# Kernel tuning notes

Hardware: AMD Instinct MI355X
Metric: run time of the kernel (lower is better)

The kernel has to match this reference:

```python
import jax, jax.numpy as jnp
import numpy as np

B, T, D_IN, EMB, H = 2, 2048, 1024, 1024, 16
HD = EMB // H  # head_dim = 64


def setup_inputs() -> dict:
    key = jax.random.key(0)
    ks = jax.random.split(key, 3)
    scale_qkv = 1.0 / np.sqrt(D_IN)
    scale_o = 1.0 / np.sqrt(EMB)
    return {
        "x": jax.random.normal(ks[0], (B, T, D_IN), dtype=jnp.float32),
        "W_qkv": jax.random.normal(ks[1], (D_IN, 3 * EMB), dtype=jnp.float32) * scale_qkv,
        "b_qkv": jnp.zeros((3 * EMB,), dtype=jnp.float32),
        "W_o": jax.random.normal(ks[2], (EMB, EMB), dtype=jnp.float32) * scale_o,
        "b_o": jnp.zeros((EMB,), dtype=jnp.float32),
    }


def reference(x, W_qkv, b_qkv, W_o, b_o):
    b, t, _ = x.shape
    qkv = x @ W_qkv + b_qkv                      # [B,T,3*EMB]
    # Match torch: reshape to (B,T,H,3*HD) -> permute -> chunk into q,k,v
    qkv = qkv.reshape(b, t, H, 3 * HD).transpose(0, 2, 1, 3)  # [B,H,T,3*HD]
    q, k, v = jnp.split(qkv, 3, axis=-1)         # each [B,H,T,HD]
    scale = 1.0 / jnp.sqrt(jnp.asarray(HD, dtype=q.dtype))
    scores = jnp.einsum("bhqd,bhkd->bhqk", q, k) * scale  # [B,H,T,T]
    attn = jax.nn.softmax(scores, axis=-1)
    values = jnp.einsum("bhqk,bhkd->bhqd", attn, v)       # [B,H,T,HD]
    values = values.transpose(0, 2, 1, 3).reshape(b, t, EMB)
    return values @ W_o + b_o
```

## Files before the change

kernel.cpp:

```cpp
#include <hip/hip_runtime.h>
#include <math.h>

typedef __bf16 bf16x8 __attribute__((ext_vector_type(8)));
typedef float f32x4 __attribute__((ext_vector_type(4)));

#define GPTR(p) ((const __attribute__((address_space(1))) void*)(p))
#define LPTR(p) ((__attribute__((address_space(3))) void*)(p))

#define QSCALE 0.18033688011112042f

__device__ __forceinline__ unsigned short f2bf(float f) {
  unsigned int u = __float_as_uint(f);
  u += 0x7FFFu + ((u >> 16) & 1u);
  return (unsigned short)(u >> 16);
}

__device__ __forceinline__ unsigned int pack_bf2(float lo, float hi) {
  return __builtin_amdgcn_perm(__float_as_uint(hi) + 0x8000u,
                               __float_as_uint(lo) + 0x8000u, 0x07060302u);
}

__device__ __forceinline__ float fast_exp2(float x) {
#if __has_builtin(__builtin_amdgcn_exp2f)
  return __builtin_amdgcn_exp2f(x);
#else
  return exp2f(x);
#endif
}

__device__ __forceinline__ f32x4 zero4() {
  f32x4 z; z[0] = 0.f; z[1] = 0.f; z[2] = 0.f; z[3] = 0.f; return z;
}

__global__ void conv_x_bf16(const float* __restrict__ in, unsigned short* __restrict__ out) {
  int i = (blockIdx.x * 256 + threadIdx.x) * 4;
  float4 v = *(const float4*)(in + i);
  ushort4 o;
  o.x = f2bf(v.x); o.y = f2bf(v.y); o.z = f2bf(v.z); o.w = f2bf(v.w);
  *(ushort4*)(out + i) = o;
}

__global__ void transpose_conv(const float* __restrict__ in, unsigned short* __restrict__ out,
                               int K, int N) {
  __shared__ float tile[64][65];
  int k0 = blockIdx.y * 64, n0 = blockIdx.x * 64;
  int t = threadIdx.x;
#pragma unroll
  for (int p = 0; p < 16; ++p) {
    int l = p * 256 + t; int r = l >> 6, c = l & 63;
    tile[r][c] = in[(size_t)(k0 + r) * N + n0 + c];
  }
  __syncthreads();
#pragma unroll
  for (int p = 0; p < 16; ++p) {
    int l = p * 256 + t; int r = l >> 6, c = l & 63;
    out[(size_t)(n0 + r) * K + k0 + c] = f2bf(tile[c][r]);
  }
}

__global__ __launch_bounds__(256) void gemm_qkv(
    const unsigned short* __restrict__ A, const unsigned short* __restrict__ Bt,
    const float* __restrict__ bias,
    unsigned short* __restrict__ Qd, unsigned short* __restrict__ Kd,
    unsigned short* __restrict__ Vtd) {
  __shared__ unsigned short As[128 * 32];
  __shared__ unsigned short Bs[128 * 32];
  const int tid = threadIdx.x, wave = tid >> 6, lane = tid & 63;
  const int quad = lane >> 4, l16 = lane & 15;
  const int wm = (wave >> 1) * 64, wn = (wave & 1) * 64;
  const int m0 = blockIdx.y * 128, n0 = blockIdx.x * 128;
  f32x4 acc[4][4];
#pragma unroll
  for (int i = 0; i < 4; ++i)
#pragma unroll
    for (int j = 0; j < 4; ++j) acc[i][j] = zero4();

  const int c = wave * 64 + lane;
  const int rA = c >> 2, o16 = (c & 3) * 8;

  for (int k0 = 0; k0 < 1024; k0 += 32) {
    __syncthreads();
    __builtin_amdgcn_global_load_lds(GPTR(A + (size_t)(m0 + rA) * 1024 + k0 + o16),
                                     LPTR(As + wave * 512), 16, 0, 0);
    __builtin_amdgcn_global_load_lds(GPTR(A + (size_t)(m0 + 64 + rA) * 1024 + k0 + o16),
                                     LPTR(As + 2048 + wave * 512), 16, 0, 0);
    __builtin_amdgcn_global_load_lds(GPTR(Bt + (size_t)(n0 + rA) * 1024 + k0 + o16),
                                     LPTR(Bs + wave * 512), 16, 0, 0);
    __builtin_amdgcn_global_load_lds(GPTR(Bt + (size_t)(n0 + 64 + rA) * 1024 + k0 + o16),
                                     LPTR(Bs + 2048 + wave * 512), 16, 0, 0);
    __syncthreads();
    bf16x8 af[4], bfr[4];
#pragma unroll
    for (int mt = 0; mt < 4; ++mt)
      af[mt] = *(const bf16x8*)(As + (wm + mt * 16 + l16) * 32 + quad * 8);
#pragma unroll
    for (int nt = 0; nt < 4; ++nt)
      bfr[nt] = *(const bf16x8*)(Bs + (wn + nt * 16 + l16) * 32 + quad * 8);
#pragma unroll
    for (int mt = 0; mt < 4; ++mt)
#pragma unroll
      for (int nt = 0; nt < 4; ++nt)
        acc[mt][nt] = __builtin_amdgcn_mfma_f32_16x16x32_bf16(af[mt], bfr[nt], acc[mt][nt], 0, 0, 0);
  }

#pragma unroll
  for (int mt = 0; mt < 4; ++mt) {
#pragma unroll
    for (int nt = 0; nt < 4; ++nt) {
      int m = m0 + wm + mt * 16 + quad * 4;
      int n = n0 + wn + nt * 16 + l16;
      float bv = bias[n];
      int h = n / 192, rem = n - h * 192;
      int which = rem >> 6, d = rem & 63;
      int b = m >> 11, t0 = m & 2047;
      size_t head = (size_t)(b * 16 + h);
      f32x4 a = acc[mt][nt];
      if (which == 0) {
        size_t base = (head * 2048 + t0) * 64 + d;
#pragma unroll
        for (int i = 0; i < 4; ++i)
          Qd[base + (size_t)i * 64] = f2bf((a[i] + bv) * QSCALE);
      } else if (which == 1) {
        size_t base = head * 131072 + (size_t)(t0 >> 6) * 4096;
#pragma unroll
        for (int i = 0; i < 4; ++i) {
          int tt = t0 + i;
          Kd[base + (tt & 63) * 64 + (((d >> 3) ^ (tt & 7)) << 3) + (d & 7)] = f2bf(a[i] + bv);
        }
      } else {
        size_t base = head * 131072 + (size_t)(t0 >> 6) * 4096;
        ushort4 o;
        o.x = f2bf(a[0] + bv); o.y = f2bf(a[1] + bv);
        o.z = f2bf(a[2] + bv); o.w = f2bf(a[3] + bv);
        *(ushort4*)(Vtd + base + d * 64 + (((((t0 & 63) >> 3)) ^ (d & 7)) << 3) + (t0 & 7)) = o;
      }
    }
  }
}

__global__ __launch_bounds__(256) void flash_attn(
    const unsigned short* __restrict__ Qg,
    const unsigned short* __restrict__ Kg,
    const unsigned short* __restrict__ Vg,
    unsigned short* __restrict__ att) {
  __shared__ unsigned short Ks[4096];
  __shared__ unsigned short Vs[4096];
  __shared__ unsigned short Ps[8192];
  const int tid = threadIdx.x, wave = tid >> 6, lane = tid & 63;
  const int quad = lane >> 4, l16 = lane & 15;
  const int h7 = l16 & 7;
  const int bh = blockIdx.y;
  const int q0 = blockIdx.x * 128 + wave * 32;

  bf16x8 bq[2][2];
#pragma unroll
  for (int qg = 0; qg < 2; ++qg)
#pragma unroll
    for (int kh = 0; kh < 2; ++kh)
      bq[qg][kh] = *(const bf16x8*)(Qg + ((size_t)bh * 2048 + q0 + qg * 16 + l16) * 64 + kh * 32 + quad * 8);

  f32x4 o[2][4];
#pragma unroll
  for (int qg = 0; qg < 2; ++qg)
#pragma unroll
    for (int i = 0; i < 4; ++i) o[qg][i] = zero4();
  float l_run[2] = {0.f, 0.f};

  unsigned short* pb = Ps + wave * 2048;
  const unsigned short* Kt = Kg + (size_t)bh * 131072;
  const unsigned short* Vt = Vg + (size_t)bh * 131072;

  for (int tile = 0; tile < 32; ++tile) {
    __syncthreads();
    const unsigned short* Kb = Kt + tile * 4096 + lane * 8;
    const unsigned short* Vb = Vt + tile * 4096 + lane * 8;
    __builtin_amdgcn_global_load_lds(GPTR(Kb + wave * 512),       LPTR(Ks + wave * 512), 16, 0, 0);
    __builtin_amdgcn_global_load_lds(GPTR(Kb + (4 + wave) * 512), LPTR(Ks + (4 + wave) * 512), 16, 0, 0);
    __builtin_amdgcn_global_load_lds(GPTR(Vb + wave * 512),       LPTR(Vs + wave * 512), 16, 0, 0);
    __builtin_amdgcn_global_load_lds(GPTR(Vb + (4 + wave) * 512), LPTR(Vs + (4 + wave) * 512), 16, 0, 0);
    __syncthreads();

    f32x4 s[2][4];
#pragma unroll
    for (int qg = 0; qg < 2; ++qg)
#pragma unroll
      for (int kt = 0; kt < 4; ++kt) s[qg][kt] = zero4();
#pragma unroll
    for (int kt = 0; kt < 4; ++kt) {
#pragma unroll
      for (int kh = 0; kh < 2; ++kh) {
        bf16x8 a = *(const bf16x8*)(Ks + (kt * 16 + l16) * 64 + (((kh * 4 + quad) ^ h7) << 3));
        s[0][kt] = __builtin_amdgcn_mfma_f32_16x16x32_bf16(a, bq[0][kh], s[0][kt], 0, 0, 0);
        s[1][kt] = __builtin_amdgcn_mfma_f32_16x16x32_bf16(a, bq[1][kh], s[1][kt], 0, 0, 0);
      }
    }

#pragma unroll
    for (int qg = 0; qg < 2; ++qg) {
      int qrow = qg * 16 + l16;
      float lsum = 0.f;
      float pv[4][4];
#pragma unroll
      for (int kt = 0; kt < 4; ++kt)
#pragma unroll
        for (int r = 0; r < 4; ++r) {
          float p = fast_exp2(s[qg][kt][r]);
          pv[kt][r] = p;
          lsum += p;
        }
#pragma unroll
      for (int kt = 0; kt < 4; ++kt) {
        uint2 pk;
        pk.x = pack_bf2(pv[kt][0], pv[kt][1]);
        pk.y = pack_bf2(pv[kt][2], pv[kt][3]);
        *(uint2*)(pb + qrow * 64 + (((2 * kt + (quad >> 1)) ^ h7) << 3) + (quad & 1) * 4) = pk;
      }
      lsum += __shfl_xor(lsum, 16);
      lsum += __shfl_xor(lsum, 32);
      l_run[qg] += lsum;
    }

#pragma unroll
    for (int st = 0; st < 2; ++st) {
      bf16x8 pf0 = *(const bf16x8*)(pb + (l16) * 64 + (((st * 4 + quad) ^ h7) << 3));
      bf16x8 pf1 = *(const bf16x8*)(pb + (16 + l16) * 64 + (((st * 4 + quad) ^ h7) << 3));
#pragma unroll
      for (int mt = 0; mt < 4; ++mt) {
        bf16x8 av = *(const bf16x8*)(Vs + (mt * 16 + l16) * 64 + (((st * 4 + quad) ^ h7) << 3));
        o[0][mt] = __builtin_amdgcn_mfma_f32_16x16x32_bf16(av, pf0, o[0][mt], 0, 0, 0);
        o[1][mt] = __builtin_amdgcn_mfma_f32_16x16x32_bf16(av, pf1, o[1][mt], 0, 0, 0);
      }
    }
  }

  int b = bh >> 4, h = bh & 15;
#pragma unroll
  for (int qg = 0; qg < 2; ++qg) {
    float inv_l = 1.f / l_run[qg];
    unsigned short* orow = att + ((size_t)b * 2048 + q0 + qg * 16 + l16) * 1024 + h * 64;
#pragma unroll
    for (int mt = 0; mt < 4; ++mt) {
      ushort4 ov;
      ov.x = f2bf(o[qg][mt][0] * inv_l);
      ov.y = f2bf(o[qg][mt][1] * inv_l);
      ov.z = f2bf(o[qg][mt][2] * inv_l);
      ov.w = f2bf(o[qg][mt][3] * inv_l);
      *(ushort4*)(orow + mt * 16 + quad * 4) = ov;
    }
  }
}

__global__ __launch_bounds__(256) void gemm_out(
    const unsigned short* __restrict__ A, const unsigned short* __restrict__ Bt,
    const float* __restrict__ bias, float* __restrict__ out) {
  __shared__ unsigned short As[128 * 32];
  __shared__ unsigned short Bs[64 * 32];
  const int tid = threadIdx.x, wave = tid >> 6, lane = tid & 63;
  const int quad = lane >> 4, l16 = lane & 15;
  const int wm = (wave >> 1) * 64, wn = (wave & 1) * 32;
  const int m0 = blockIdx.y * 128, n0 = blockIdx.x * 64;
  f32x4 acc[4][2];
#pragma unroll
  for (int i = 0; i < 4; ++i)
#pragma unroll
    for (int j = 0; j < 2; ++j) acc[i][j] = zero4();

  const int c = wave * 64 + lane;
  const int rA = c >> 2, o16 = (c & 3) * 8;

  for (int k0 = 0; k0 < 1024; k0 += 32) {
    __syncthreads();
    __builtin_amdgcn_global_load_lds(GPTR(A + (size_t)(m0 + rA) * 1024 + k0 + o16),
                                     LPTR(As + wave * 512), 16, 0, 0);
    __builtin_amdgcn_global_load_lds(GPTR(A + (size_t)(m0 + 64 + rA) * 1024 + k0 + o16),
                                     LPTR(As + 2048 + wave * 512), 16, 0, 0);
    __builtin_amdgcn_global_load_lds(GPTR(Bt + (size_t)(n0 + rA) * 1024 + k0 + o16),
                                     LPTR(Bs + wave * 512), 16, 0, 0);
    __syncthreads();
    bf16x8 af[4], bfr[2];
#pragma unroll
    for (int mt = 0; mt < 4; ++mt)
      af[mt] = *(const bf16x8*)(As + (wm + mt * 16 + l16) * 32 + quad * 8);
#pragma unroll
    for (int nt = 0; nt < 2; ++nt)
      bfr[nt] = *(const bf16x8*)(Bs + (wn + nt * 16 + l16) * 32 + quad * 8);
#pragma unroll
    for (int mt = 0; mt < 4; ++mt)
#pragma unroll
      for (int nt = 0; nt < 2; ++nt)
        acc[mt][nt] = __builtin_amdgcn_mfma_f32_16x16x32_bf16(af[mt], bfr[nt], acc[mt][nt], 0, 0, 0);
  }

#pragma unroll
  for (int mt = 0; mt < 4; ++mt) {
#pragma unroll
    for (int nt = 0; nt < 2; ++nt) {
      int m = m0 + wm + mt * 16 + quad * 4;
      int n = n0 + wn + nt * 16 + l16;
      float bv = bias[n];
      float* orow = out + (size_t)m * 1024 + n;
      orow[0]        = acc[mt][nt][0] + bv;
      orow[1024]     = acc[mt][nt][1] + bv;
      orow[2 * 1024] = acc[mt][nt][2] + bv;
      orow[3 * 1024] = acc[mt][nt][3] + bv;
    }
  }
}

extern "C" void kernel_launch(void* const* d_in, const int* in_sizes, int n_in,
                              void* d_out, int out_size, void* d_ws, size_t ws_size,
                              hipStream_t stream) {
  const float* x    = (const float*)d_in[0];
  const float* Wqkv = (const float*)d_in[1];
  const float* bqkv = (const float*)d_in[2];
  const float* Wo   = (const float*)d_in[3];
  const float* bo   = (const float*)d_in[4];
  float* out = (float*)d_out;

  unsigned short* xb    = (unsigned short*)d_ws;
  unsigned short* wqkvt = xb    + (size_t)4096 * 1024;
  unsigned short* wot   = wqkvt + (size_t)3072 * 1024;
  unsigned short* Qd    = wot   + (size_t)1024 * 1024;
  unsigned short* Kd    = Qd    + (size_t)32 * 2048 * 64;
  unsigned short* Vtd   = Kd    + (size_t)32 * 2048 * 64;
  unsigned short* attb  = Vtd   + (size_t)32 * 2048 * 64;

  conv_x_bf16<<<4096, 256, 0, stream>>>(x, xb);
  transpose_conv<<<dim3(48, 16), 256, 0, stream>>>(Wqkv, wqkvt, 1024, 3072);
  transpose_conv<<<dim3(16, 16), 256, 0, stream>>>(Wo, wot, 1024, 1024);
  gemm_qkv<<<dim3(24, 32), 256, 0, stream>>>(xb, wqkvt, bqkv, Qd, Kd, Vtd);
  flash_attn<<<dim3(16, 32), 256, 0, stream>>>(Qd, Kd, Vtd, attb);
  gemm_out<<<dim3(16, 32), 256, 0, stream>>>(attb, wot, bo, out);
}
```

Measured before the change: 215.2 us.

## Double-buffer K/V tiles in flash attention to overlap loads with compute

```diff
diff --git a/kernel.cpp b/kernel.cpp
--- a/kernel.cpp
+++ b/kernel.cpp
@@ -143,8 +143,8 @@
     const unsigned short* __restrict__ Kg,
     const unsigned short* __restrict__ Vg,
     unsigned short* __restrict__ att) {
-  __shared__ unsigned short Ks[4096];
-  __shared__ unsigned short Vs[4096];
+  __shared__ unsigned short Ks[2][4096];
+  __shared__ unsigned short Vs[2][4096];
   __shared__ unsigned short Ps[8192];
   const int tid = threadIdx.x, wave = tid >> 6, lane = tid & 63;
   const int quad = lane >> 4, l16 = lane & 15;
@@ -167,18 +167,26 @@
   float l_run[2] = {0.f, 0.f};
 
   unsigned short* pb = Ps + wave * 2048;
-  const unsigned short* Kt = Kg + (size_t)bh * 131072;
-  const unsigned short* Vt = Vg + (size_t)bh * 131072;
-
+  const unsigned short* Kt = Kg + (size_t)bh * 131072 + lane * 8;
+  const unsigned short* Vt = Vg + (size_t)bh * 131072 + lane * 8;
+  const int so0 = wave * 512, so1 = (4 + wave) * 512;
+
+#define STAGE_KV(buf, tile)                                                              \
+  do {                                                                                   \
+    const unsigned short* Kb_ = Kt + (tile) * 4096;                                      \
+    const unsigned short* Vb_ = Vt + (tile) * 4096;                                      \
+    __builtin_amdgcn_global_load_lds(GPTR(Kb_ + so0), LPTR(&Ks[buf][so0]), 16, 0, 0);    \
+    __builtin_amdgcn_global_load_lds(GPTR(Kb_ + so1), LPTR(&Ks[buf][so1]), 16, 0, 0);    \
+    __builtin_amdgcn_global_load_lds(GPTR(Vb_ + so0), LPTR(&Vs[buf][so0]), 16, 0, 0);    \
+    __builtin_amdgcn_global_load_lds(GPTR(Vb_ + so1), LPTR(&Vs[buf][so1]), 16, 0, 0);    \
+  } while (0)
+
+  STAGE_KV(0, 0);
+  __syncthreads();
+
+  int cur = 0;
   for (int tile = 0; tile < 32; ++tile) {
-    __syncthreads();
-    const unsigned short* Kb = Kt + tile * 4096 + lane * 8;
-    const unsigned short* Vb = Vt + tile * 4096 + lane * 8;
-    __builtin_amdgcn_global_load_lds(GPTR(Kb + wave * 512),       LPTR(Ks + wave * 512), 16, 0, 0);
-    __builtin_amdgcn_global_load_lds(GPTR(Kb + (4 + wave) * 512), LPTR(Ks + (4 + wave) * 512), 16, 0, 0);
-    __builtin_amdgcn_global_load_lds(GPTR(Vb + wave * 512),       LPTR(Vs + wave * 512), 16, 0, 0);
-    __builtin_amdgcn_global_load_lds(GPTR(Vb + (4 + wave) * 512), LPTR(Vs + (4 + wave) * 512), 16, 0, 0);
-    __syncthreads();
+    if (tile < 31) STAGE_KV(cur ^ 1, tile + 1);
 
     f32x4 s[2][4];
 #pragma unroll
@@ -189,7 +197,7 @@
     for (int kt = 0; kt < 4; ++kt) {
 #pragma unroll
       for (int kh = 0; kh < 2; ++kh) {
-        bf16x8 a = *(const bf16x8*)(Ks + (kt * 16 + l16) * 64 + (((kh * 4 + quad) ^ h7) << 3));
+        bf16x8 a = *(const bf16x8*)(&Ks[cur][(kt * 16 + l16) * 64 + (((kh * 4 + quad) ^ h7) << 3)]);
         s[0][kt] = __builtin_amdgcn_mfma_f32_16x16x32_bf16(a, bq[0][kh], s[0][kt], 0, 0, 0);
         s[1][kt] = __builtin_amdgcn_mfma_f32_16x16x32_bf16(a, bq[1][kh], s[1][kt], 0, 0, 0);
       }
@@ -226,12 +234,16 @@
       bf16x8 pf1 = *(const bf16x8*)(pb + (16 + l16) * 64 + (((st * 4 + quad) ^ h7) << 3));
 #pragma unroll
       for (int mt = 0; mt < 4; ++mt) {
-        bf16x8 av = *(const bf16x8*)(Vs + (mt * 16 + l16) * 64 + (((st * 4 + quad) ^ h7) << 3));
+        bf16x8 av = *(const bf16x8*)(&Vs[cur][(mt * 16 + l16) * 64 + (((st * 4 + quad) ^ h7) << 3)]);
         o[0][mt] = __builtin_amdgcn_mfma_f32_16x16x32_bf16(av, pf0, o[0][mt], 0, 0, 0);
         o[1][mt] = __builtin_amdgcn_mfma_f32_16x16x32_bf16(av, pf1, o[1][mt], 0, 0, 0);
       }
     }
-  }
+
+    __syncthreads();
+    cur ^= 1;
+  }
+#undef STAGE_KV
 
   int b = bh >> 4, h = bh & 15;
 #pragma unroll
```

New measurement: 214.5 us. Within noise of the previous version (-0.3%).

## Double-buffer per-wave K/V tiles and keep P in registers via permlane swaps

Applied to the files above, without the earlier changes.

```diff
diff --git a/kernel.cpp b/kernel.cpp
--- a/kernel.cpp
+++ b/kernel.cpp
@@ -15,9 +15,10 @@
   return (unsigned short)(u >> 16);
 }
 
-__device__ __forceinline__ unsigned int pack_bf2(float lo, float hi) {
-  return __builtin_amdgcn_perm(__float_as_uint(hi) + 0x8000u,
-                               __float_as_uint(lo) + 0x8000u, 0x07060302u);
+__device__ __forceinline__ unsigned int cvtpk_bf16(float lo, float hi) {
+  unsigned int r;
+  asm("v_cvt_pk_bf16_f32 %0, %1, %2" : "=v"(r) : "v"(lo), "v"(hi));
+  return r;
 }
 
 __device__ __forceinline__ float fast_exp2(float x) {
@@ -30,6 +31,13 @@
 
 __device__ __forceinline__ f32x4 zero4() {
   f32x4 z; z[0] = 0.f; z[1] = 0.f; z[2] = 0.f; z[3] = 0.f; return z;
+}
+
+__device__ __forceinline__ void permlane_swap32(unsigned int& a, unsigned int& b) {
+  asm("v_permlane32_swap_b32 %0, %1" : "+v"(a), "+v"(b));
+}
+__device__ __forceinline__ void permlane_swap16(unsigned int& a, unsigned int& b) {
+  asm("v_permlane16_swap_b32 %0, %1" : "+v"(a), "+v"(b));
 }
 
 __global__ void conv_x_bf16(const float* __restrict__ in, unsigned short* __restrict__ out) {
@@ -128,11 +136,13 @@
           Kd[base + (tt & 63) * 64 + (((d >> 3) ^ (tt & 7)) << 3) + (d & 7)] = f2bf(a[i] + bv);
         }
       } else {
-        size_t base = head * 131072 + (size_t)(t0 >> 6) * 4096;
+        int rr = d & 31;
+        int cc = ((d >> 5) << 2) + ((t0 & 31) >> 3);
+        size_t base = head * 131072 + (size_t)(t0 >> 5) * 2048;
         ushort4 o;
         o.x = f2bf(a[0] + bv); o.y = f2bf(a[1] + bv);
         o.z = f2bf(a[2] + bv); o.w = f2bf(a[3] + bv);
-        *(ushort4*)(Vtd + base + d * 64 + (((((t0 & 63) >> 3)) ^ (d & 7)) << 3) + (t0 & 7)) = o;
+        *(ushort4*)(Vtd + base + rr * 64 + (((cc ^ (rr & 7))) << 3) + (t0 & 7)) = o;
       }
     }
   }
@@ -143,9 +153,7 @@
     const unsigned short* __restrict__ Kg,
     const unsigned short* __restrict__ Vg,
     unsigned short* __restrict__ att) {
-  __shared__ unsigned short Ks[4096];
-  __shared__ unsigned short Vs[4096];
-  __shared__ unsigned short Ps[8192];
+  __shared__ unsigned short S[4][4][2048];
   const int tid = threadIdx.x, wave = tid >> 6, lane = tid & 63;
   const int quad = lane >> 4, l16 = lane & 15;
   const int h7 = l16 & 7;
@@ -166,71 +174,86 @@
     for (int i = 0; i < 4; ++i) o[qg][i] = zero4();
   float l_run[2] = {0.f, 0.f};
 
-  unsigned short* pb = Ps + wave * 2048;
-  const unsigned short* Kt = Kg + (size_t)bh * 131072;
-  const unsigned short* Vt = Vg + (size_t)bh * 131072;
-
-  for (int tile = 0; tile < 32; ++tile) {
-    __syncthreads();
-    const unsigned short* Kb = Kt + tile * 4096 + lane * 8;
-    const unsigned short* Vb = Vt + tile * 4096 + lane * 8;
-    __builtin_amdgcn_global_load_lds(GPTR(Kb + wave * 512),       LPTR(Ks + wave * 512), 16, 0, 0);
-    __builtin_amdgcn_global_load_lds(GPTR(Kb + (4 + wave) * 512), LPTR(Ks + (4 + wave) * 512), 16, 0, 0);
-    __builtin_amdgcn_global_load_lds(GPTR(Vb + wave * 512),       LPTR(Vs + wave * 512), 16, 0, 0);
-    __builtin_amdgcn_global_load_lds(GPTR(Vb + (4 + wave) * 512), LPTR(Vs + (4 + wave) * 512), 16, 0, 0);
-    __syncthreads();
-
-    f32x4 s[2][4];
-#pragma unroll
-    for (int qg = 0; qg < 2; ++qg)
-#pragma unroll
-      for (int kt = 0; kt < 4; ++kt) s[qg][kt] = zero4();
-#pragma unroll
-    for (int kt = 0; kt < 4; ++kt) {
-#pragma unroll
-      for (int kh = 0; kh < 2; ++kh) {
-        bf16x8 a = *(const bf16x8*)(Ks + (kt * 16 + l16) * 64 + (((kh * 4 + quad) ^ h7) << 3));
-        s[0][kt] = __builtin_amdgcn_mfma_f32_16x16x32_bf16(a, bq[0][kh], s[0][kt], 0, 0, 0);
-        s[1][kt] = __builtin_amdgcn_mfma_f32_16x16x32_bf16(a, bq[1][kh], s[1][kt], 0, 0, 0);
-      }
-    }
-
-#pragma unroll
-    for (int qg = 0; qg < 2; ++qg) {
-      int qrow = qg * 16 + l16;
-      float lsum = 0.f;
-      float pv[4][4];
-#pragma unroll
-      for (int kt = 0; kt < 4; ++kt)
-#pragma unroll
-        for (int r = 0; r < 4; ++r) {
-          float p = fast_exp2(s[qg][kt][r]);
-          pv[kt][r] = p;
-          lsum += p;
-        }
-#pragma unroll
-      for (int kt = 0; kt < 4; ++kt) {
-        uint2 pk;
-        pk.x = pack_bf2(pv[kt][0], pv[kt][1]);
-        pk.y = pack_bf2(pv[kt][2], pv[kt][3]);
-        *(uint2*)(pb + qrow * 64 + (((2 * kt + (quad >> 1)) ^ h7) << 3) + (quad & 1) * 4) = pk;
-      }
-      lsum += __shfl_xor(lsum, 16);
-      lsum += __shfl_xor(lsum, 32);
-      l_run[qg] += lsum;
-    }
-
-#pragma unroll
-    for (int st = 0; st < 2; ++st) {
-      bf16x8 pf0 = *(const bf16x8*)(pb + (l16) * 64 + (((st * 4 + quad) ^ h7) << 3));
-      bf16x8 pf1 = *(const bf16x8*)(pb + (16 + l16) * 64 + (((st * 4 + quad) ^ h7) << 3));
-#pragma unroll
-      for (int mt = 0; mt < 4; ++mt) {
-        bf16x8 av = *(const bf16x8*)(Vs + (mt * 16 + l16) * 64 + (((st * 4 + quad) ^ h7) << 3));
-        o[0][mt] = __builtin_amdgcn_mfma_f32_16x16x32_bf16(av, pf0, o[0][mt], 0, 0, 0);
-        o[1][mt] = __builtin_amdgcn_mfma_f32_16x16x32_bf16(av, pf1, o[1][mt], 0, 0, 0);
-      }
-    }
+  const unsigned short* Kt = Kg + (size_t)bh * 131072 + lane * 8;
+  const unsigned short* Vt = Vg + (size_t)bh * 131072 + lane * 8;
+  unsigned short* Wb = &S[wave][0][0];
+  unsigned short* Wl = Wb + lane * 8;
+
+#define STAGE(B, TILE)                                                                    \
+  do {                                                                                    \
+    const unsigned short* ks_ = Kt + (size_t)(TILE) * 2048;                               \
+    const unsigned short* vs_ = Vt + (size_t)(TILE) * 2048;                               \
+    __builtin_amdgcn_global_load_lds(GPTR(ks_),        LPTR(Wl + (B) * 2048),        16, 0, 0); \
+    __builtin_amdgcn_global_load_lds(GPTR(ks_ + 512),  LPTR(Wl + (B) * 2048 + 512),  16, 0, 0); \
+    __builtin_amdgcn_global_load_lds(GPTR(ks_ + 1024), LPTR(Wl + (B) * 2048 + 1024), 16, 0, 0); \
+    __builtin_amdgcn_global_load_lds(GPTR(ks_ + 1536), LPTR(Wl + (B) * 2048 + 1536), 16, 0, 0); \
+    __builtin_amdgcn_global_load_lds(GPTR(vs_),        LPTR(Wl + (2 + (B)) * 2048),        16, 0, 0); \
+    __builtin_amdgcn_global_load_lds(GPTR(vs_ + 512),  LPTR(Wl + (2 + (B)) * 2048 + 512),  16, 0, 0); \
+    __builtin_amdgcn_global_load_lds(GPTR(vs_ + 1024), LPTR(Wl + (2 + (B)) * 2048 + 1024), 16, 0, 0); \
+    __builtin_amdgcn_global_load_lds(GPTR(vs_ + 1536), LPTR(Wl + (2 + (B)) * 2048 + 1536), 16, 0, 0); \
+  } while (0)
+
+#define BODY(CUR, LAST)                                                                   \
+  do {                                                                                    \
+    int ntile_ = (tile + 1) & 63;                                                         \
+    if (!(LAST)) {                                                                        \
+      asm volatile("s_waitcnt lgkmcnt(0)" ::: "memory");    \
+      STAGE((CUR) ^ 1, ntile_);                                                           \
+      asm volatile("s_waitcnt vmcnt(8)" ::: "memory");       \
+    } else {                                                                              \
+      asm volatile("s_waitcnt vmcnt(0)" ::: "memory");                                    \
+    }                                                                                     \
+    const unsigned short* Kb_ = Wb + (CUR) * 2048;                                        \
+    const unsigned short* Vb_ = Wb + (2 + (CUR)) * 2048;                                  \
+    f32x4 s_[2][2];                                                                       \
+    s_[0][0] = zero4(); s_[0][1] = zero4(); s_[1][0] = zero4(); s_[1][1] = zero4();       \
+    _Pragma("unroll")                                                                     \
+    for (int kt = 0; kt < 2; ++kt) {                                                      \
+      _Pragma("unroll")                                                                   \
+      for (int kh = 0; kh < 2; ++kh) {                                                    \
+        bf16x8 a_ = *(const bf16x8*)(Kb_ + (kt * 16 + l16) * 64 + (((kh * 4 + quad) ^ h7) << 3)); \
+        s_[0][kt] = __builtin_amdgcn_mfma_f32_16x16x32_bf16(a_, bq[0][kh], s_[0][kt], 0, 0, 0); \
+        s_[1][kt] = __builtin_amdgcn_mfma_f32_16x16x32_bf16(a_, bq[1][kh], s_[1][kt], 0, 0, 0); \
+      }                                                                                   \
+    }                                                                                     \
+    bf16x8 pf_[2];                                                                        \
+    _Pragma("unroll")                                                                     \
+    for (int qg = 0; qg < 2; ++qg) {                                                      \
+      float p00 = fast_exp2(s_[qg][0][0]), p01 = fast_exp2(s_[qg][0][1]);                 \
+      float p02 = fast_exp2(s_[qg][0][2]), p03 = fast_exp2(s_[qg][0][3]);                 \
+      float p10 = fast_exp2(s_[qg][1][0]), p11 = fast_exp2(s_[qg][1][1]);                 \
+      float p12 = fast_exp2(s_[qg][1][2]), p13 = fast_exp2(s_[qg][1][3]);                 \
+      l_run[qg] += ((p00 + p01) + (p02 + p03)) + ((p10 + p11) + (p12 + p13));             \
+      unsigned int a0 = cvtpk_bf16(p00, p01), a1 = cvtpk_bf16(p02, p03);                  \
+      unsigned int b0 = cvtpk_bf16(p10, p11), b1 = cvtpk_bf16(p12, p13);                  \
+      permlane_swap32(a0, b0); permlane_swap16(a0, b0);                                   \
+      permlane_swap32(a1, b1); permlane_swap16(a1, b1);                                   \
+      union { unsigned int u[4]; bf16x8 v; } x_;                                          \
+      x_.u[0] = a0; x_.u[1] = a1; x_.u[2] = b0; x_.u[3] = b1;                             \
+      pf_[qg] = x_.v;                                                                     \
+    }                                                                                     \
+    _Pragma("unroll")                                                                     \
+    for (int mt = 0; mt < 4; ++mt) {                                                      \
+      bf16x8 av_ = *(const bf16x8*)(Vb_ + ((mt & 1) * 16 + l16) * 64 + ((((mt >> 1) * 4 + quad) ^ h7) << 3)); \
+      o[0][mt] = __builtin_amdgcn_mfma_f32_16x16x32_bf16(av_, pf_[0], o[0][mt], 0, 0, 0); \
+      o[1][mt] = __builtin_amdgcn_mfma_f32_16x16x32_bf16(av_, pf_[1], o[1][mt], 0, 0, 0); \
+    }                                                                                     \
+    tile = ntile_;                                                                        \
+  } while (0)
+
+  int tile = ((wave << 4) + ((blockIdx.x & 3) << 2)) & 63;
+  STAGE(0, tile);
+  for (int it = 0; it < 32; ++it) {
+    BODY(0, false);
+    BODY(1, it == 31);
+  }
+#undef BODY
+#undef STAGE
+
+#pragma unroll
+  for (int qg = 0; qg < 2; ++qg) {
+    l_run[qg] += __shfl_xor(l_run[qg], 16);
+    l_run[qg] += __shfl_xor(l_run[qg], 32);
   }
 
   int b = bh >> 4, h = bh & 15;
```

After: 241.8 us. 12.4% more time.
